# Kernel optimization log

Measured on AMD Instinct MI355X. Metric: run time of the kernel, lower is better.

## Reference

```python
import jax, jax.numpy as jnp
import numpy as np

MAX_DIM = 1024
VOCAB = 257
DEPTH = 6
Q_DIM = MAX_DIM // 4  # 256
EXP_DIMS = [1, 2, 4, 8, 16, 32, 64, 128]  # expander sizes: current_q doubles up to Q_DIM
BATCH, SEQ = 8, 4096


def qlinear(q, W):
    """Quaternion Hamilton-product linear.
    q: [..., in, 4] (last dim = r,i,j,k components), W: [4, out, in] (stacked r,i,j,k weights).
    Returns [..., out, 4].
    """
    # P[..., o, w, a] = F.linear(component_a, W_w)  -> all 16 small GEMMs in one einsum
    P = jnp.einsum('...ia,woi->...owa', q, W)
    Pr, Pi, Pj, Pk = P[..., 0, :], P[..., 1, :], P[..., 2, :], P[..., 3, :]  # each [..., out, 4]
    out_r = Pr[..., 0] - Pi[..., 1] - Pj[..., 2] - Pk[..., 3]
    out_i = Pi[..., 0] + Pr[..., 1] + Pk[..., 2] - Pj[..., 3]
    out_j = Pj[..., 0] - Pk[..., 1] + Pr[..., 2] + Pi[..., 3]
    out_k = Pk[..., 0] + Pj[..., 1] - Pi[..., 2] + Pr[..., 3]
    return jnp.stack([out_r, out_i, out_j, out_k], axis=-1)


def qnormalize(q):
    norm = jnp.linalg.norm(q, axis=-1, keepdims=True)
    return q / (norm + 1e-8)


def setup_inputs() -> dict:
    key = jax.random.key(0)
    ks = jax.random.split(key, 4 + len(EXP_DIMS))
    inp = {}
    inp['x'] = jax.random.randint(ks[0], (BATCH, SEQ), 0, VOCAB)
    inp['emb'] = jax.random.normal(ks[1], (VOCAB, 4), dtype=jnp.float32)
    for idx, cq in enumerate(EXP_DIMS):
        scale = cq ** (-0.5)
        inp[f'w_exp{idx}'] = jax.random.uniform(ks[2 + idx], (4, cq, cq), jnp.float32, -scale, scale)
    scale = Q_DIM ** (-0.5)
    inp['w_layers'] = jax.random.uniform(ks[-2], (DEPTH, 4, Q_DIM, Q_DIM), jnp.float32, -scale, scale)
    inp['w_head'] = jax.random.normal(ks[-1], (VOCAB, MAX_DIM), dtype=jnp.float32) * MAX_DIM ** (-0.5)
    return inp


def reference(x, emb, w_exp0, w_exp1, w_exp2, w_exp3, w_exp4, w_exp5, w_exp6, w_exp7,
              w_layers, w_head):
    q = emb[x][:, :, None, :]  # [B, S, 1, 4]
    for w in (w_exp0, w_exp1, w_exp2, w_exp3, w_exp4, w_exp5, w_exp6, w_exp7):
        delta = jnp.tanh(qlinear(q, w))
        q = jnp.concatenate([q + delta, q - delta], axis=2)  # doubles quaternion dim
    for d in range(DEPTH):
        q = qnormalize(qlinear(q, w_layers[d]))
    stability_loss = jnp.mean(jnp.abs(q[..., 0]))
    h_flat = q.reshape(x.shape[0], x.shape[1], -1)  # [B, S, MAX_DIM]
    logits = jnp.einsum('bsd,vd->bsv', h_flat, w_head)
    return (logits, stability_loss)
```

## Files before the change

kernel.cpp:

```cpp
#include <hip/hip_runtime.h>


typedef _Float16 f16x8 __attribute__((ext_vector_type(8)));
typedef float    f32x4 __attribute__((ext_vector_type(4)));

#define GL2LDS16(gp, lp) __builtin_amdgcn_global_load_lds(                     \
    (const __attribute__((address_space(1))) void*)(gp),                       \
    (__attribute__((address_space(3))) void*)(lp), 16, 0, 0)

__device__ __forceinline__ unsigned short f2h(float f) {
  union { _Float16 h; unsigned short u; } c;
  c.h = (_Float16)f;
  return c.u;
}
__device__ __forceinline__ float h2f(unsigned short u) {
  union { unsigned short u; _Float16 h; } c;
  c.u = u;
  return (float)c.h;
}

__global__ __launch_bounds__(256) void expand_ham(
    const float* __restrict__ w, unsigned short* __restrict__ out,
    int cq, int kbits, int total) {
  int id = blockIdx.x * 256 + threadIdx.x;
  if (id >= total) return;
  const int K = 1 << kbits;
  const int n = id >> kbits;
  const int k = id & (K - 1);
  float val = 0.f;
  if (n < 4 * cq) {
    const int o = n >> 2, a = n & 3, i = k >> 2, b = k & 3;
    const int   comp[4][4] = {{0,1,2,3},{1,0,3,2},{2,3,0,1},{3,2,1,0}};
    const float sgn [4][4] = {{1.f,-1.f,-1.f,-1.f},{1.f,1.f,1.f,-1.f},
                              {1.f,-1.f,1.f,1.f},{1.f,1.f,-1.f,1.f}};
    val = sgn[a][b] * w[comp[a][b] * cq * cq + o * cq + i];
  }
  out[id] = f2h(val);
}

__global__ __launch_bounds__(256) void conv_head(
    const float* __restrict__ wh, unsigned short* __restrict__ out) {
  int id = blockIdx.x * 256 + threadIdx.x;
  int v = id >> 10, k = id & 1023;
  out[id] = f2h(v < 257 ? wh[v * 1024 + k] : 0.f);
}

template <int CQ>
__device__ __forceinline__ void exp_step(float (&q)[16][4],
                                         const float* __restrict__ w) {
  float d[CQ][4];
#pragma unroll
  for (int o = 0; o < CQ; o++) {
    float pr = 0.f, pi = 0.f, pj = 0.f, pk = 0.f;
#pragma unroll
    for (int i = 0; i < CQ; i++) {
      const float wr = w[0 * CQ * CQ + o * CQ + i];
      const float wi = w[1 * CQ * CQ + o * CQ + i];
      const float wj = w[2 * CQ * CQ + o * CQ + i];
      const float wk = w[3 * CQ * CQ + o * CQ + i];
      const float qr = q[i][0], qi = q[i][1], qj = q[i][2], qk = q[i][3];
      pr += wr * qr - wi * qi - wj * qj - wk * qk;
      pi += wi * qr + wr * qi + wk * qj - wj * qk;
      pj += wj * qr - wk * qi + wr * qj + wi * qk;
      pk += wk * qr + wj * qi - wi * qj + wr * qk;
    }
    d[o][0] = tanhf(pr); d[o][1] = tanhf(pi);
    d[o][2] = tanhf(pj); d[o][3] = tanhf(pk);
  }
#pragma unroll
  for (int o = 0; o < CQ; o++)
#pragma unroll
    for (int a = 0; a < 4; a++) {
      const float dd = d[o][a], qq = q[o][a];
      q[o][a]      = qq + dd;
      q[CQ + o][a] = qq - dd;
    }
}

__global__ __launch_bounds__(256) void embed_expand(
    const int* __restrict__ x, const float* __restrict__ emb,
    const float* __restrict__ w0, const float* __restrict__ w1,
    const float* __restrict__ w2, const float* __restrict__ w3,
    unsigned short* __restrict__ out) {
  const int t = blockIdx.x * 256 + threadIdx.x;
  float q[16][4];
  const int v = x[t];
  const float4 e = *(const float4*)(emb + v * 4);
  q[0][0] = e.x; q[0][1] = e.y; q[0][2] = e.z; q[0][3] = e.w;
  exp_step<1>(q, w0);
  exp_step<2>(q, w1);
  exp_step<4>(q, w2);
  exp_step<8>(q, w3);
  ushort4* o4 = (ushort4*)(out + (size_t)t * 64);
#pragma unroll
  for (int c = 0; c < 16; c++) {
    ushort4 u;
    u.x = f2h(q[c][0]); u.y = f2h(q[c][1]);
    u.z = f2h(q[c][2]); u.w = f2h(q[c][3]);
    o4[c] = u;
  }
}

template <int EPI>
__global__ __launch_bounds__(256) void gemm_epi(
    const unsigned short* __restrict__ W,
    const unsigned short* __restrict__ Act,
    unsigned short* __restrict__ OutB, float* __restrict__ OutF,
    int K, int Nreal, int ldout) {
  __shared__ unsigned short WtL[128 * 32];
  __shared__ unsigned short WtH[128 * 32];
  __shared__ unsigned short AtL[128 * 32];
  __shared__ unsigned short AtH[128 * 32];

  const int tid  = threadIdx.x;
  const int wave = tid >> 6;
  const int lane = tid & 63;
  const int l15  = lane & 15;
  const int quad = lane >> 4;

  const int Gx = gridDim.x;
  const int L  = blockIdx.y * Gx + blockIdx.x;
  const int j  = L & 7;
  const int s  = L >> 3;
  const int nblock = (s % Gx) * 128;
  const int mblock = (32 * j + s / Gx) * 128;
  const int wn = (wave & 1) * 64;
  const int wm = (wave >> 1) * 64;

  f32x4 acc[4][4];
  const f32x4 zero = {0.f, 0.f, 0.f, 0.f};
#pragma unroll
  for (int a = 0; a < 4; a++)
#pragma unroll
    for (int b = 0; b < 4; b++) acc[a][b] = zero;

  const int row0 = tid >> 2;
  const int sub  = tid & 3;
  const unsigned short* gW0 = W   + (size_t)(nblock + row0)      * K + sub * 8;
  const unsigned short* gW1 = W   + (size_t)(nblock + row0 + 64) * K + sub * 8;
  const unsigned short* gA0 = Act + (size_t)(mblock + row0)      * K + sub * 8;
  const unsigned short* gA1 = Act + (size_t)(mblock + row0 + 64) * K + sub * 8;
  unsigned short* lWL0 = &WtL[wave * 512];
  unsigned short* lWL1 = &WtL[2048 + wave * 512];
  unsigned short* lWH0 = &WtH[wave * 512];
  unsigned short* lWH1 = &WtH[2048 + wave * 512];
  unsigned short* lAL0 = &AtL[wave * 512];
  unsigned short* lAL1 = &AtL[2048 + wave * 512];
  unsigned short* lAH0 = &AtH[wave * 512];
  unsigned short* lAH1 = &AtH[2048 + wave * 512];

  for (int kb = 0; kb < K; kb += 64) {
    GL2LDS16(gW0 + kb,      lWL0);
    GL2LDS16(gW1 + kb,      lWL1);
    GL2LDS16(gW0 + kb + 32, lWH0);
    GL2LDS16(gW1 + kb + 32, lWH1);
    GL2LDS16(gA0 + kb,      lAL0);
    GL2LDS16(gA1 + kb,      lAL1);
    GL2LDS16(gA0 + kb + 32, lAH0);
    GL2LDS16(gA1 + kb + 32, lAH1);
    __syncthreads();

    {
      f16x8 afr[4], bfr[4];
#pragma unroll
      for (int tn = 0; tn < 4; tn++)
        afr[tn] = *(const f16x8*)&WtL[(wn + tn * 16 + l15) * 32 + quad * 8];
#pragma unroll
      for (int tm = 0; tm < 4; tm++)
        bfr[tm] = *(const f16x8*)&AtL[(wm + tm * 16 + l15) * 32 + quad * 8];
#pragma unroll
      for (int tn = 0; tn < 4; tn++)
#pragma unroll
        for (int tm = 0; tm < 4; tm++)
          acc[tn][tm] = __builtin_amdgcn_mfma_f32_16x16x32_f16(
              afr[tn], bfr[tm], acc[tn][tm], 0, 0, 0);
    }
    {
      f16x8 afr[4], bfr[4];
#pragma unroll
      for (int tn = 0; tn < 4; tn++)
        afr[tn] = *(const f16x8*)&WtH[(wn + tn * 16 + l15) * 32 + quad * 8];
#pragma unroll
      for (int tm = 0; tm < 4; tm++)
        bfr[tm] = *(const f16x8*)&AtH[(wm + tm * 16 + l15) * 32 + quad * 8];
#pragma unroll
      for (int tn = 0; tn < 4; tn++)
#pragma unroll
        for (int tm = 0; tm < 4; tm++)
          acc[tn][tm] = __builtin_amdgcn_mfma_f32_16x16x32_f16(
              afr[tn], bfr[tm], acc[tn][tm], 0, 0, 0);
    }
    __syncthreads();
  }

#pragma unroll
  for (int tn = 0; tn < 4; tn++) {
    const int n = nblock + wn + tn * 16 + quad * 4;
    if (n < Nreal) {
#pragma unroll
      for (int tm = 0; tm < 4; tm++) {
        const int token = mblock + wm + tm * 16 + l15;
        const f32x4 v = acc[tn][tm];
        const unsigned short* ip = Act + (size_t)token * K + n;
        const float i0 = h2f(ip[0]), i1 = h2f(ip[1]);
        const float i2 = h2f(ip[2]), i3 = h2f(ip[3]);
        const float d0 = tanhf(v[0]), d1 = tanhf(v[1]);
        const float d2 = tanhf(v[2]), d3 = tanhf(v[3]);
        ushort4 up, um;
        up.x = f2h(i0 + d0); up.y = f2h(i1 + d1);
        up.z = f2h(i2 + d2); up.w = f2h(i3 + d3);
        um.x = f2h(i0 - d0); um.y = f2h(i1 - d1);
        um.z = f2h(i2 - d2); um.w = f2h(i3 - d3);
        *(ushort4*)&OutB[(size_t)token * ldout + n] = up;
        *(ushort4*)&OutB[(size_t)token * ldout + Nreal + n] = um;
      }
    }
  }
}

template <int EPI>
__global__ __launch_bounds__(512, 2) void gemm8p(
    const unsigned short* __restrict__ W,
    const unsigned short* __restrict__ Act,
    unsigned short* __restrict__ OutB, float* __restrict__ OutF,
    int K, int NW) {
  __shared__ unsigned short S[65536];
  __shared__ float lsum[8];

  const int tid  = threadIdx.x;
  const int wave = tid >> 6;
  const int lane = tid & 63;
  const int l15  = lane & 15;
  const int quad = lane >> 4;
  const int wr   = wave >> 2;
  const int wc   = wave & 3;

  const int Gx = gridDim.x;
  const int L  = blockIdx.y * Gx + blockIdx.x;
  const int j  = L & 7;
  const int s  = L >> 3;
  const int mtile = j * (gridDim.y >> 3) + s / Gx;
  const int ntile = s % Gx;
  const int nblock = ntile * 256;
  const int mblock = mtile * 256;

  const int NT = K >> 5;

  f32x4 acc[8][4];
  const f32x4 zero = {0.f, 0.f, 0.f, 0.f};
#pragma unroll
  for (int a = 0; a < 8; a++)
#pragma unroll
    for (int b = 0; b < 4; b++) acc[a][b] = zero;

  const int rA = tid >> 2;
  const int sl = (tid & 3) ^ ((tid >> 3) & 3);
  const int w0r = nblock + rA;
  const int w1r = nblock + 128 + rA;
  const int cw0 = w0r < NW ? w0r : NW - 1;
  const int cw1 = w1r < NW ? w1r : NW - 1;
  const unsigned short* sW0 = W   + (size_t)cw0 * K + sl * 8;
  const unsigned short* sW1 = W   + (size_t)cw1 * K + sl * 8;
  const unsigned short* sA0 = Act + (size_t)(mblock + rA)       * K + sl * 8;
  const unsigned short* sA1 = Act + (size_t)(mblock + 128 + rA) * K + sl * 8;

  const int swz = (quad * 8) ^ ((l15 & 6) << 2);

  for (int t = 0; t < 3 && t < NT; ++t) {
    const int kb = t * 32;
    unsigned short* d = S + t * 16384 + tid * 8;
    GL2LDS16(sW0 + kb, d);
    GL2LDS16(sA0 + kb, d + 8192);
    GL2LDS16(sW1 + kb, d + 4096);
    GL2LDS16(sA1 + kb, d + 12288);
  }
  if (NT >= 3)      asm volatile("s_waitcnt vmcnt(8)" ::: "memory");
  else if (NT == 2) asm volatile("s_waitcnt vmcnt(4)" ::: "memory");
  else              asm volatile("s_waitcnt vmcnt(0)" ::: "memory");
  __builtin_amdgcn_s_barrier();

  for (int kt = 0; kt < NT; ++kt) {
    const unsigned short* SA = S + (kt & 3) * 16384;
    const unsigned short* SB = SA + 8192;
    const int  nxt = (kt + 3) & 3;
    const bool pf  = (kt + 3) < NT;
    const int  kb  = (kt + 3) * 32;
    unsigned short* d = S + nxt * 16384 + tid * 8;

    f16x8 af[4], bf[4];
#pragma unroll
    for (int t4 = 0; t4 < 4; t4++)
      af[t4] = *(const f16x8*)(SA + (wr * 128 + t4 * 16 + l15) * 32 + swz);
#pragma unroll
    for (int t4 = 0; t4 < 4; t4++)
      bf[t4] = *(const f16x8*)(SB + (wc * 64 + t4 * 16 + l15) * 32 + swz);
    if (pf) { GL2LDS16(sW0 + kb, d); GL2LDS16(sA0 + kb, d + 8192); }
    __builtin_amdgcn_s_barrier();
    asm volatile("s_waitcnt lgkmcnt(0)" ::: "memory");
    __builtin_amdgcn_sched_barrier(0);
    __builtin_amdgcn_s_setprio(1);
#pragma unroll
    for (int tn = 0; tn < 4; tn++)
#pragma unroll
      for (int tm = 0; tm < 4; tm++)
        acc[tn][tm] = __builtin_amdgcn_mfma_f32_16x16x32_f16(
            af[tn], bf[tm], acc[tn][tm], 0, 0, 0);
    __builtin_amdgcn_s_setprio(0);
    __builtin_amdgcn_s_barrier();
#pragma unroll
    for (int t4 = 0; t4 < 4; t4++)
      af[t4] = *(const f16x8*)(SA + (wr * 128 + 64 + t4 * 16 + l15) * 32 + swz);
    if (pf) { GL2LDS16(sW1 + kb, d + 4096); GL2LDS16(sA1 + kb, d + 12288); }
    __builtin_amdgcn_s_barrier();
    asm volatile("s_waitcnt lgkmcnt(0)" ::: "memory");
    __builtin_amdgcn_sched_barrier(0);
    __builtin_amdgcn_s_setprio(1);
#pragma unroll
    for (int tn = 0; tn < 4; tn++)
#pragma unroll
      for (int tm = 0; tm < 4; tm++)
        acc[4 + tn][tm] = __builtin_amdgcn_mfma_f32_16x16x32_f16(
            af[tn], bf[tm], acc[4 + tn][tm], 0, 0, 0);
    __builtin_amdgcn_s_setprio(0);
    if (kt < NT - 1) {
      if (kt + 3 < NT)       asm volatile("s_waitcnt vmcnt(8)" ::: "memory");
      else if (kt + 3 == NT) asm volatile("s_waitcnt vmcnt(4)" ::: "memory");
      else                   asm volatile("s_waitcnt vmcnt(0)" ::: "memory");
      __builtin_amdgcn_s_barrier();
    }
  }

  if constexpr (EPI == 1 || EPI == 2) {
    float loss = 0.f;
#pragma unroll
    for (int tn = 0; tn < 8; tn++) {
      const int n = nblock + wr * 128 + tn * 16 + quad * 4;
#pragma unroll
      for (int tm = 0; tm < 4; tm++) {
        const int token = mblock + wc * 64 + tm * 16 + l15;
        const f32x4 v = acc[tn][tm];
        const float nrm =
            sqrtf(v[0] * v[0] + v[1] * v[1] + v[2] * v[2] + v[3] * v[3]);
        const float inv = 1.f / (nrm + 1e-8f);
        ushort4 u;
        u.x = f2h(v[0] * inv); u.y = f2h(v[1] * inv);
        u.z = f2h(v[2] * inv); u.w = f2h(v[3] * inv);
        *(ushort4*)&OutB[(size_t)token * 1024 + n] = u;
        if constexpr (EPI == 2) loss += fabsf(v[0] * inv);
      }
    }
    if constexpr (EPI == 2) {
#pragma unroll
      for (int off = 32; off > 0; off >>= 1) loss += __shfl_down(loss, off);
      if (lane == 0) lsum[wave] = loss;
      __syncthreads();
      if (tid == 0) {
        float t = 0.f;
#pragma unroll
        for (int w8 = 0; w8 < 8; w8++) t += lsum[w8];
        atomicAdd(OutF, t * (1.f / 8388608.f));
      }
    }
  } else {
#pragma unroll
    for (int tn = 0; tn < 8; tn++) {
      const int n = nblock + wr * 128 + tn * 16 + quad * 4;
      if (n < 257) {
#pragma unroll
        for (int tm = 0; tm < 4; tm++) {
          const int token = mblock + wc * 64 + tm * 16 + l15;
          const f32x4 v = acc[tn][tm];
#pragma unroll
          for (int r = 0; r < 4; r++)
            if (n + r < 257) OutF[(size_t)token * 257 + n + r] = v[r];
        }
      }
    }
  }
}

extern "C" void kernel_launch(void* const* d_in, const int* in_sizes, int n_in,
                              void* d_out, int out_size, void* d_ws,
                              size_t ws_size, hipStream_t stream) {
  const int*   x    = (const int*)d_in[0];
  const float* emb  = (const float*)d_in[1];
  const float* we0  = (const float*)d_in[2];
  const float* we1  = (const float*)d_in[3];
  const float* we2  = (const float*)d_in[4];
  const float* we3  = (const float*)d_in[5];
  const float* we4  = (const float*)d_in[6];
  const float* we5  = (const float*)d_in[7];
  const float* we6  = (const float*)d_in[8];
  const float* we7  = (const float*)d_in[9];
  const float* wlay = (const float*)d_in[10];
  const float* wh   = (const float*)d_in[11];
  float* out = (float*)d_out;

  char* p = (char*)d_ws;
  auto alloc = [&](size_t bytes) {
    void* r = (void*)p;
    p += (bytes + 255) & ~(size_t)255;
    return r;
  };
  unsigned short* act0 = (unsigned short*)alloc(32768ull * 1024 * 2);
  unsigned short* act1 = (unsigned short*)alloc(32768ull * 1024 * 2);
  unsigned short* E4 = (unsigned short*)alloc(128 * 64 * 2);
  unsigned short* E5 = (unsigned short*)alloc(128 * 128 * 2);
  unsigned short* E6 = (unsigned short*)alloc(256 * 256 * 2);
  unsigned short* E7 = (unsigned short*)alloc(512 * 512 * 2);
  unsigned short* EL = (unsigned short*)alloc(6ull * 1024 * 1024 * 2);
  unsigned short* WH = (unsigned short*)alloc(384 * 1024 * 2);

  hipMemsetAsync(out + 8421376, 0, 4, stream);

  expand_ham<<<dim3(8192 / 256), 256, 0, stream>>>(we4, E4, 16, 6, 128 * 64);
  expand_ham<<<dim3(16384 / 256), 256, 0, stream>>>(we5, E5, 32, 7, 128 * 128);
  expand_ham<<<dim3(65536 / 256), 256, 0, stream>>>(we6, E6, 64, 8, 256 * 256);
  expand_ham<<<dim3(262144 / 256), 256, 0, stream>>>(we7, E7, 128, 9,
                                                     512 * 512);
  for (int d = 0; d < 6; d++)
    expand_ham<<<dim3(1048576 / 256), 256, 0, stream>>>(
        wlay + (size_t)d * 262144, EL + (size_t)d * 1048576, 256, 10, 1048576);
  conv_head<<<dim3(384 * 1024 / 256), 256, 0, stream>>>(wh, WH);

  embed_expand<<<dim3(128), 256, 0, stream>>>(x, emb, we0, we1, we2, we3, act0);

  gemm_epi<0><<<dim3(1, 256), 256, 0, stream>>>(E4, act0, act1, nullptr, 64,
                                                64, 128);
  gemm_epi<0><<<dim3(1, 256), 256, 0, stream>>>(E5, act1, act0, nullptr, 128,
                                                128, 256);
  gemm_epi<0><<<dim3(2, 256), 256, 0, stream>>>(E6, act0, act1, nullptr, 256,
                                                256, 512);
  gemm_epi<0><<<dim3(4, 256), 256, 0, stream>>>(E7, act1, act0, nullptr, 512,
                                                512, 1024);

  unsigned short* a = act0;
  unsigned short* b = act1;
  for (int d = 0; d < 5; d++) {
    gemm8p<1><<<dim3(4, 128), 512, 0, stream>>>(EL + (size_t)d * 1048576, a, b,
                                                nullptr, 1024, 1024);
    unsigned short* t = a; a = b; b = t;
  }
  gemm8p<2><<<dim3(4, 128), 512, 0, stream>>>(EL + 5ull * 1048576, a, b,
                                              out + 8421376, 1024, 1024);
  { unsigned short* t = a; a = b; b = t; }

  gemm8p<3><<<dim3(2, 128), 512, 0, stream>>>(WH, a, nullptr, out, 1024, 384);
}
```

Before: 819.8 us.

## Restructure gemm8p main loop sync and route expander GEMMs through it

The gemm8p main loop drops the two mid-iteration barriers and lgkmcnt waits. Global-to-LDS prefetches are issued first, and the second A-fragment goes into a separate register set so its LDS reads can overlap the first MFMA batch. A new EPI==0 epilogue (tanh plus residual, written as +/- halves) lets the last two expander stages use the 256x256-tile 512-thread gemm8p instead of gemm_epi. This trades fewer synchronisation points and larger tiles for more register pressure. Removing the barriers also risks an LDS race, since prefetches now target the slot that other waves may still be reading.

```diff
diff --git a/kernel.cpp b/kernel.cpp
--- a/kernel.cpp
+++ b/kernel.cpp
@@ -223,7 +223,7 @@
     const unsigned short* __restrict__ W,
     const unsigned short* __restrict__ Act,
     unsigned short* __restrict__ OutB, float* __restrict__ OutF,
-    int K, int NW) {
+    int K, int NW, int ldout) {
   __shared__ unsigned short S[65536];
   __shared__ float lsum[8];
 
@@ -278,6 +278,7 @@
   else if (NT == 2) asm volatile("s_waitcnt vmcnt(4)" ::: "memory");
   else              asm volatile("s_waitcnt vmcnt(0)" ::: "memory");
   __builtin_amdgcn_s_barrier();
+  __builtin_amdgcn_sched_barrier(0);
 
   for (int kt = 0; kt < NT; ++kt) {
     const unsigned short* SA = S + (kt & 3) * 16384;
@@ -287,17 +288,15 @@
     const int  kb  = (kt + 3) * 32;
     unsigned short* d = S + nxt * 16384 + tid * 8;
 
+    if (pf) { GL2LDS16(sW0 + kb, d); GL2LDS16(sA0 + kb, d + 8192); }
+
     f16x8 af[4], bf[4];
+#pragma unroll
+    for (int t4 = 0; t4 < 4; t4++)
+      bf[t4] = *(const f16x8*)(SB + (wc * 64 + t4 * 16 + l15) * 32 + swz);
 #pragma unroll
     for (int t4 = 0; t4 < 4; t4++)
       af[t4] = *(const f16x8*)(SA + (wr * 128 + t4 * 16 + l15) * 32 + swz);
-#pragma unroll
-    for (int t4 = 0; t4 < 4; t4++)
-      bf[t4] = *(const f16x8*)(SB + (wc * 64 + t4 * 16 + l15) * 32 + swz);
-    if (pf) { GL2LDS16(sW0 + kb, d); GL2LDS16(sA0 + kb, d + 8192); }
-    __builtin_amdgcn_s_barrier();
-    asm volatile("s_waitcnt lgkmcnt(0)" ::: "memory");
-    __builtin_amdgcn_sched_barrier(0);
     __builtin_amdgcn_s_setprio(1);
 #pragma unroll
     for (int tn = 0; tn < 4; tn++)
@@ -306,31 +305,54 @@
         acc[tn][tm] = __builtin_amdgcn_mfma_f32_16x16x32_f16(
             af[tn], bf[tm], acc[tn][tm], 0, 0, 0);
     __builtin_amdgcn_s_setprio(0);
-    __builtin_amdgcn_s_barrier();
+
+    if (pf) { GL2LDS16(sW1 + kb, d + 4096); GL2LDS16(sA1 + kb, d + 12288); }
+
+    f16x8 ah[4];
 #pragma unroll
     for (int t4 = 0; t4 < 4; t4++)
-      af[t4] = *(const f16x8*)(SA + (wr * 128 + 64 + t4 * 16 + l15) * 32 + swz);
-    if (pf) { GL2LDS16(sW1 + kb, d + 4096); GL2LDS16(sA1 + kb, d + 12288); }
-    __builtin_amdgcn_s_barrier();
-    asm volatile("s_waitcnt lgkmcnt(0)" ::: "memory");
-    __builtin_amdgcn_sched_barrier(0);
+      ah[t4] = *(const f16x8*)(SA + (wr * 128 + 64 + t4 * 16 + l15) * 32 + swz);
     __builtin_amdgcn_s_setprio(1);
 #pragma unroll
     for (int tn = 0; tn < 4; tn++)
 #pragma unroll
       for (int tm = 0; tm < 4; tm++)
         acc[4 + tn][tm] = __builtin_amdgcn_mfma_f32_16x16x32_f16(
-            af[tn], bf[tm], acc[4 + tn][tm], 0, 0, 0);
+            ah[tn], bf[tm], acc[4 + tn][tm], 0, 0, 0);
     __builtin_amdgcn_s_setprio(0);
+
     if (kt < NT - 1) {
       if (kt + 3 < NT)       asm volatile("s_waitcnt vmcnt(8)" ::: "memory");
       else if (kt + 3 == NT) asm volatile("s_waitcnt vmcnt(4)" ::: "memory");
       else                   asm volatile("s_waitcnt vmcnt(0)" ::: "memory");
       __builtin_amdgcn_s_barrier();
-    }
-  }
-
-  if constexpr (EPI == 1 || EPI == 2) {
+      __builtin_amdgcn_sched_barrier(0);
+    }
+  }
+
+  if constexpr (EPI == 0) {
+#pragma unroll
+    for (int tn = 0; tn < 8; tn++) {
+      const int n = nblock + wr * 128 + tn * 16 + quad * 4;
+#pragma unroll
+      for (int tm = 0; tm < 4; tm++) {
+        const int token = mblock + wc * 64 + tm * 16 + l15;
+        const f32x4 v = acc[tn][tm];
+        const unsigned short* ip = Act + (size_t)token * K + n;
+        const float i0 = h2f(ip[0]), i1 = h2f(ip[1]);
+        const float i2 = h2f(ip[2]), i3 = h2f(ip[3]);
+        const float d0 = tanhf(v[0]), d1 = tanhf(v[1]);
+        const float d2 = tanhf(v[2]), d3 = tanhf(v[3]);
+        ushort4 up, um;
+        up.x = f2h(i0 + d0); up.y = f2h(i1 + d1);
+        up.z = f2h(i2 + d2); up.w = f2h(i3 + d3);
+        um.x = f2h(i0 - d0); um.y = f2h(i1 - d1);
+        um.z = f2h(i2 - d2); um.w = f2h(i3 - d3);
+        *(ushort4*)&OutB[(size_t)token * ldout + n] = up;
+        *(ushort4*)&OutB[(size_t)token * ldout + NW + n] = um;
+      }
+    }
+  } else if constexpr (EPI == 1 || EPI == 2) {
     float loss = 0.f;
 #pragma unroll
     for (int tn = 0; tn < 8; tn++) {
@@ -429,21 +451,22 @@
                                                 64, 128);
   gemm_epi<0><<<dim3(1, 256), 256, 0, stream>>>(E5, act1, act0, nullptr, 128,
                                                 128, 256);
-  gemm_epi<0><<<dim3(2, 256), 256, 0, stream>>>(E6, act0, act1, nullptr, 256,
-                                                256, 512);
-  gemm_epi<0><<<dim3(4, 256), 256, 0, stream>>>(E7, act1, act0, nullptr, 512,
-                                                512, 1024);
+  gemm8p<0><<<dim3(1, 128), 512, 0, stream>>>(E6, act0, act1, nullptr, 256,
+                                              256, 512);
+  gemm8p<0><<<dim3(2, 128), 512, 0, stream>>>(E7, act1, act0, nullptr, 512,
+                                              512, 1024);
 
   unsigned short* a = act0;
   unsigned short* b = act1;
   for (int d = 0; d < 5; d++) {
     gemm8p<1><<<dim3(4, 128), 512, 0, stream>>>(EL + (size_t)d * 1048576, a, b,
-                                                nullptr, 1024, 1024);
+                                                nullptr, 1024, 1024, 1024);
     unsigned short* t = a; a = b; b = t;
   }
   gemm8p<2><<<dim3(4, 128), 512, 0, stream>>>(EL + 5ull * 1048576, a, b,
-                                              out + 8421376, 1024, 1024);
+                                              out + 8421376, 1024, 1024, 1024);
   { unsigned short* t = a; a = b; b = t; }
 
-  gemm8p<3><<<dim3(2, 128), 512, 0, stream>>>(WH, a, nullptr, out, 1024, 384);
-}
+  gemm8p<3><<<dim3(2, 128), 512, 0, stream>>>(WH, a, nullptr, out, 1024, 384,
+                                              0);
+}
```

New measurement: 995.2 us. 21.4% more time.
